# Performance work log

Hardware: AMD Instinct MI355X
Metric: run time of the kernel (lower is better)

The kernel has to match this reference:

```python
import jax, jax.numpy as jnp
import numpy as np

N_NODES = 100000
N_EDGES = 1600000
F_IN, H1, H2 = 128, 64, 32


def spmm(src, dst, edge_weight, x, n_nodes):
    # A @ x with A in COO form: out[dst] += w * x[src]
    msgs = x[src] * edge_weight[:, None]          # [E, d] gather + scale
    return jax.ops.segment_sum(msgs, dst, num_segments=n_nodes)


def setup_inputs() -> dict:
    key = jax.random.key(0)
    k1, k2, k3, k4, k5, k6 = jax.random.split(key, 6)
    features = jax.random.normal(k1, (N_NODES, F_IN), dtype=jnp.float32)
    # positive weights, roughly 1/deg scale as in a normalized adjacency
    edge_weight = jax.random.uniform(k2, (N_EDGES,), dtype=jnp.float32) * 0.125
    W1 = jax.random.normal(k3, (F_IN, H1), dtype=jnp.float32) * (1.0 / np.sqrt(F_IN))
    W2 = jax.random.normal(k4, (H1, H2), dtype=jnp.float32) * (1.0 / np.sqrt(H1))
    src = jax.random.randint(k5, (N_EDGES,), 0, N_NODES, dtype=jnp.int64 if jax.config.jax_enable_x64 else jnp.int32)
    dst = jax.random.randint(k6, (N_EDGES,), 0, N_NODES, dtype=jnp.int64 if jax.config.jax_enable_x64 else jnp.int32)
    return {"features": features, "edge_weight": edge_weight, "W1": W1, "W2": W2,
            "src": src, "dst": dst}


def reference(features, edge_weight, W1, W2, src, dst):
    # Layer 1: relu(A @ (X W1)); dropout is identity (eval mode / rate 0)
    h1 = jax.nn.relu(spmm(src, dst, edge_weight, features @ W1, N_NODES))  # [N, H1]
    # Layer 2: A @ (h1 W2)
    embeddings = spmm(src, dst, edge_weight, h1 @ W2, N_NODES)             # [N, H2]
    return embeddings
```

## Files before the change

### kernel.cpp

```cpp
#include <hip/hip_runtime.h>
#include <hip/hip_fp16.h>


constexpr int N_NODES = 100000;
constexpr int N_EDGES = 1600000;
constexpr int F_IN = 128;
constexpr int H1 = 64;
constexpr int H2 = 32;
constexpr int BSHIFT = 9;
constexpr int BNODES = 1 << BSHIFT;
constexpr int NBUCK = (N_NODES + BNODES - 1) / BNODES;
constexpr int CAP = 10240;
constexpr int CHUNK = 4096;
constexpr int P1_WGS = (N_EDGES + CHUNK - 1) / CHUNK;
constexpr int GEMM_WGS = (N_NODES + 255) / 256;

__global__ __launch_bounds__(256) void init_cursors(int* __restrict__ cursor)
{
    int t = threadIdx.x;
    if (t < NBUCK) cursor[t] = t * CAP;
}

__global__ __launch_bounds__(256) void pass1_bin_gemm1(
    const int* __restrict__ src, const int* __restrict__ dst,
    const float* __restrict__ w, int* __restrict__ cursor,
    int2* __restrict__ staging,
    const float* __restrict__ X, const float* __restrict__ W1,
    __half* __restrict__ xw1out)
{
    __shared__ float smem[F_IN * H1];

    if (blockIdx.x < GEMM_WGS) {
        for (int i = threadIdx.x; i < F_IN * H1; i += 256) smem[i] = W1[i];
        __syncthreads();
        int row = blockIdx.x * 256 + threadIdx.x;
        if (row >= N_NODES) return;
        const float4* xr = reinterpret_cast<const float4*>(X + (size_t)row * F_IN);
        float4 acc[H1 / 4];
#pragma unroll
        for (int j = 0; j < H1 / 4; ++j) acc[j] = make_float4(0.f, 0.f, 0.f, 0.f);
        for (int k4 = 0; k4 < F_IN / 4; ++k4) {
            float4 xv = xr[k4];
#pragma unroll
            for (int kk = 0; kk < 4; ++kk) {
                float xk = (kk == 0) ? xv.x : (kk == 1) ? xv.y
                         : (kk == 2) ? xv.z : xv.w;
                const float4* wr = reinterpret_cast<const float4*>(
                    &smem[(k4 * 4 + kk) * H1]);
#pragma unroll
                for (int j = 0; j < H1 / 4; ++j) {
                    float4 wv = wr[j];
                    acc[j].x += xk * wv.x;
                    acc[j].y += xk * wv.y;
                    acc[j].z += xk * wv.z;
                    acc[j].w += xk * wv.w;
                }
            }
        }
        __half2* oh = reinterpret_cast<__half2*>(xw1out + (size_t)row * H1);
#pragma unroll
        for (int j = 0; j < H1 / 4; ++j) {
            oh[j * 2 + 0] = __floats2half2_rn(acc[j].x, acc[j].y);
            oh[j * 2 + 1] = __floats2half2_rn(acc[j].z, acc[j].w);
        }
        return;
    }

    int* lcnt  = (int*)smem;
    int* lbase = lcnt + 256;

    int e0 = (blockIdx.x - GEMM_WGS) * CHUNK;
    int nhere = N_EDGES - e0; if (nhere > CHUNK) nhere = CHUNK;

    lcnt[threadIdx.x] = 0;
    __syncthreads();

    int   es[16];
    int   ed[16];
    float ew[16];
    {
        bool v = (threadIdx.x * 16) < nhere;
        int tb = e0 + threadIdx.x * 16;
        if (v) {
            const int4* sp = reinterpret_cast<const int4*>(src + tb);
            const int4* dp = reinterpret_cast<const int4*>(dst + tb);
            const float4* wp = reinterpret_cast<const float4*>(w + tb);
#pragma unroll
            for (int q = 0; q < 4; ++q) {
                int4 sv = sp[q], dv = dp[q]; float4 wv = wp[q];
                es[4*q+0]=sv.x; es[4*q+1]=sv.y; es[4*q+2]=sv.z; es[4*q+3]=sv.w;
                ed[4*q+0]=dv.x; ed[4*q+1]=dv.y; ed[4*q+2]=dv.z; ed[4*q+3]=dv.w;
                ew[4*q+0]=wv.x; ew[4*q+1]=wv.y; ew[4*q+2]=wv.z; ew[4*q+3]=wv.w;
            }
        } else {
#pragma unroll
            for (int k = 0; k < 16; ++k) { es[k]=0; ed[k]=-1; ew[k]=0.f; }
        }
    }
#pragma unroll
    for (int k = 0; k < 16; ++k)
        if (ed[k] >= 0) atomicAdd(&lcnt[ed[k] >> BSHIFT], 1);
    __syncthreads();
    if (threadIdx.x < NBUCK) {
        int c = lcnt[threadIdx.x];
        lbase[threadIdx.x] = (c > 0) ? atomicAdd(&cursor[threadIdx.x], c) : 0;
    }
    __syncthreads();
    lcnt[threadIdx.x] = 0;
    __syncthreads();
#pragma unroll
    for (int k = 0; k < 16; ++k) {
        if (ed[k] >= 0) {
            int b = ed[k] >> BSHIFT;
            int r = atomicAdd(&lcnt[b], 1);
            int pos = lbase[b] + r;
            if (pos < (b + 1) * CAP)
                staging[pos] = make_int2(
                    es[k] | ((ed[k] & (BNODES - 1)) << 17),
                    __float_as_int(ew[k]));
        }
    }
}

__global__ __launch_bounds__(1024) void sort_bucket(
    const int* __restrict__ cursor, const int2* __restrict__ staging,
    int2* __restrict__ csr, int2* __restrict__ seg)
{
    __shared__ int  lcnt[BNODES];
    __shared__ int  lofs[BNODES];
    __shared__ int2 sorted[CAP];
    __shared__ int  total_sh;

    int b = blockIdx.x, t = threadIdx.x;
    int base = b * CAP;
    int cnt = cursor[b] - base; if (cnt > CAP) cnt = CAP;

    if (t < BNODES) lcnt[t] = 0;
    __syncthreads();

    for (int j = t; j < cnt; j += 1024)
        atomicAdd(&lcnt[(staging[base + j].x >> 17) & (BNODES - 1)], 1);
    __syncthreads();

    int v = (t < BNODES) ? lcnt[t] : 0;
    int pc = (v + 3) & ~3;
    if (t < BNODES) lofs[t] = pc;
    __syncthreads();
    for (int off = 1; off < BNODES; off <<= 1) {
        int add = (t >= off && t < BNODES) ? lofs[t - off] : 0;
        __syncthreads();
        if (t < BNODES) lofs[t] += add;
        __syncthreads();
    }
    if (t < BNODES) {
        int pexcl = lofs[t] - pc;
        seg[b * BNODES + t] = make_int2(base + pexcl, pc);
        lcnt[t] = pexcl;
        for (int j = v; j < pc; ++j)
            if (pexcl + j < CAP) sorted[pexcl + j] = make_int2(0, 0);
        if (t == BNODES - 1) {
            int tot = lofs[t]; if (tot > CAP) tot = CAP;
            total_sh = tot;
        }
    }
    __syncthreads();

    for (int j = t; j < cnt; j += 1024) {
        int2 c = staging[base + j];
        int node = (c.x >> 17) & (BNODES - 1);
        int pos = atomicAdd(&lcnt[node], 1);
        if (pos < CAP) sorted[pos] = make_int2(c.x & 0x1FFFF, c.y);
    }
    __syncthreads();

    int total = total_sh;
    for (int j = t; j < total; j += 1024) csr[base + j] = sorted[j];
}

__global__ __launch_bounds__(256) void spmm1_fused(
    const int2* __restrict__ seg, const int2* __restrict__ csr,
    const __half* __restrict__ xin, const float* __restrict__ W2,
    __half* __restrict__ h1w2h)
{
    int gid = blockIdx.x * 256 + threadIdx.x;
    int node = __builtin_amdgcn_readfirstlane(gid >> 6);
    int f = gid & 63;
    int par = f >> 5;
    int f2 = f & 31;

    float w2r[32];
#pragma unroll
    for (int kk = 0; kk < 32; ++kk)
        w2r[kk] = W2[(par * 32 + kk) * H2 + f2];

    int2 s = seg[node];
    int start = __builtin_amdgcn_readfirstlane(s.x);
    int cntp  = __builtin_amdgcn_readfirstlane(s.y);
    const int4* csr4 = reinterpret_cast<const int4*>(csr);

    float2 a0 = make_float2(0.f, 0.f), a1 = make_float2(0.f, 0.f);
    for (int e = start; e < start + cntp; e += 4) {
        int4 p0 = csr4[(e >> 1) + 0];
        int4 p1 = csr4[(e >> 1) + 1];
        int  sA = par ? p0.z : p0.x;
        float wA = __int_as_float(par ? p0.w : p0.y);
        int  sB = par ? p1.z : p1.x;
        float wB = __int_as_float(par ? p1.w : p1.y);
        float2 xA = __half22float2(
            *reinterpret_cast<const __half2*>(&xin[(size_t)sA * H1 + 2 * f2]));
        float2 xB = __half22float2(
            *reinterpret_cast<const __half2*>(&xin[(size_t)sB * H1 + 2 * f2]));
        a0.x += wA * xA.x; a0.y += wA * xA.y;
        a1.x += wB * xB.x; a1.y += wB * xB.y;
    }
    float rx = a0.x + a1.x, ry = a0.y + a1.y;
    rx += __shfl_xor(rx, 32, 64);
    ry += __shfl_xor(ry, 32, 64);
    rx = fmaxf(rx, 0.f); ry = fmaxf(ry, 0.f);

    float o = 0.f;
#pragma unroll
    for (int kk = 0; kk < 32; kk += 2) {
        int p = 16 * par + (kk >> 1);
        o += __shfl(rx, p, 64) * w2r[kk];
        o += __shfl(ry, p, 64) * w2r[kk + 1];
    }
    o += __shfl_xor(o, 32, 64);
    if (f < 32)
        h1w2h[(size_t)node * H2 + f2] = __float2half(o);
}

__global__ __launch_bounds__(256) void spmm_csr32h(
    const int2* __restrict__ seg, const int2* __restrict__ csr,
    const __half* __restrict__ xin, float* __restrict__ out)
{
    int gid = blockIdx.x * 256 + threadIdx.x;
    int node = __builtin_amdgcn_readfirstlane(gid >> 6);
    int lane = gid & 63;
    int slot = lane >> 4;
    int f2 = lane & 15;

    int2 s = seg[node];
    int start = __builtin_amdgcn_readfirstlane(s.x);
    int cntp  = __builtin_amdgcn_readfirstlane(s.y);
    int endp = start + cntp;
    const int4* csr4 = reinterpret_cast<const int4*>(csr);

    float2 a0 = make_float2(0.f, 0.f), a1 = make_float2(0.f, 0.f);
    int e = start;
    for (; e + 8 <= endp; e += 8) {
        int4 q0 = csr4[(e >> 1) + 0];
        int4 q1 = csr4[(e >> 1) + 1];
        int4 q2 = csr4[(e >> 1) + 2];
        int4 q3 = csr4[(e >> 1) + 3];
        int4 qa = (slot & 2) ? q1 : q0;
        int  sA = (slot & 1) ? qa.z : qa.x;
        float wA = __int_as_float((slot & 1) ? qa.w : qa.y);
        int4 qb = (slot & 2) ? q3 : q2;
        int  sB = (slot & 1) ? qb.z : qb.x;
        float wB = __int_as_float((slot & 1) ? qb.w : qb.y);
        float2 xA = __half22float2(
            *reinterpret_cast<const __half2*>(&xin[(size_t)sA * H2 + 2 * f2]));
        float2 xB = __half22float2(
            *reinterpret_cast<const __half2*>(&xin[(size_t)sB * H2 + 2 * f2]));
        a0.x += wA * xA.x; a0.y += wA * xA.y;
        a1.x += wB * xB.x; a1.y += wB * xB.y;
    }
    if (e < endp) {
        int4 q0 = csr4[(e >> 1) + 0];
        int4 q1 = csr4[(e >> 1) + 1];
        int4 qa = (slot & 2) ? q1 : q0;
        int  sA = (slot & 1) ? qa.z : qa.x;
        float wA = __int_as_float((slot & 1) ? qa.w : qa.y);
        float2 xA = __half22float2(
            *reinterpret_cast<const __half2*>(&xin[(size_t)sA * H2 + 2 * f2]));
        a0.x += wA * xA.x; a0.y += wA * xA.y;
    }
    float ox = a0.x + a1.x, oy = a0.y + a1.y;
    ox += __shfl_xor(ox, 16, 64); oy += __shfl_xor(oy, 16, 64);
    ox += __shfl_xor(ox, 32, 64); oy += __shfl_xor(oy, 32, 64);
    if (lane < 16)
        *reinterpret_cast<float2*>(&out[(size_t)node * H2 + 2 * f2]) =
            make_float2(ox, oy);
}

extern "C" void kernel_launch(void* const* d_in, const int* in_sizes, int n_in,
                              void* d_out, int out_size, void* d_ws, size_t ws_size,
                              hipStream_t stream)
{
    const float* features    = (const float*)d_in[0];
    const float* edge_weight = (const float*)d_in[1];
    const float* W1          = (const float*)d_in[2];
    const float* W2          = (const float*)d_in[3];
    const int*   src         = (const int*)d_in[4];
    const int*   dst         = (const int*)d_in[5];
    float* out = (float*)d_out;

    char* p = (char*)d_ws;
    __half* xw1h   = (__half*)p;    p += (size_t)N_NODES * H1 * 2;
    __half* h1w2h  = (__half*)p;    p += (size_t)N_NODES * H2 * 2;
    int2*  staging = (int2*)p;      p += (size_t)NBUCK * CAP * 8;
    int2*  csr     = (int2*)p;      p += (size_t)NBUCK * CAP * 8;
    int2*  seg     = (int2*)p;      p += (size_t)NBUCK * BNODES * 8;
    int*   cursor  = (int*)p;       p += 256 * 4;

    init_cursors<<<1, 256, 0, stream>>>(cursor);
    pass1_bin_gemm1<<<P1_WGS + GEMM_WGS, 256, 0, stream>>>(
        src, dst, edge_weight, cursor, staging, features, W1, xw1h);
    sort_bucket<<<NBUCK, 1024, 0, stream>>>(cursor, staging, csr, seg);

    spmm1_fused<<<(N_NODES * 64) / 256, 256, 0, stream>>>(seg, csr, xw1h, W2, h1w2h);
    spmm_csr32h<<<(N_NODES * 64) / 256, 256, 0, stream>>>(seg, csr, h1w2h, out);
}
```

Measured before the change: 158.0 us.

## Restructure layer-1 SpMM into persistent waves with four-edge slots and 8-byte gathers

The fused layer-1 SpMM kernel now runs as a persistent grid of 8192 blocks, where each wave loops over many nodes instead of one wave per node. Inside a wave, lanes split into four edge slots of 16 lanes, and each lane gathers 4 halves (8 bytes) per edge, so 8 edges are processed per iteration instead of 4. A tail path handles leftover edges. The aim is fewer, wider gather loads and an amortised W2 register load, at the cost of an extra cross-slot shuffle reduction and a shuffle-heavy W2 product.

```diff
diff --git a/kernel.cpp b/kernel.cpp
--- a/kernel.cpp
+++ b/kernel.cpp
@@ -14,6 +14,8 @@
 constexpr int CHUNK = 4096;
 constexpr int P1_WGS = (N_EDGES + CHUNK - 1) / CHUNK;
 constexpr int GEMM_WGS = (N_NODES + 255) / 256;
+constexpr int SP1_BLOCKS = 8192;
+constexpr int SP1_WAVES = SP1_BLOCKS * 4;
 
 __global__ __launch_bounds__(256) void init_cursors(int* __restrict__ cursor)
 {
@@ -182,52 +184,84 @@
     const __half* __restrict__ xin, const float* __restrict__ W2,
     __half* __restrict__ h1w2h)
 {
-    int gid = blockIdx.x * 256 + threadIdx.x;
-    int node = __builtin_amdgcn_readfirstlane(gid >> 6);
-    int f = gid & 63;
-    int par = f >> 5;
-    int f2 = f & 31;
+    int tid = blockIdx.x * 256 + threadIdx.x;
+    int wave0 = tid >> 6;
+    int f = tid & 63;
+    int slot = f >> 4;
+    int fq = f & 15;
+    int j = f & 31;
+    int khalf = f >> 5;
+    int shalf = slot >> 1;
+    int spar = slot & 1;
 
     float w2r[32];
 #pragma unroll
     for (int kk = 0; kk < 32; ++kk)
-        w2r[kk] = W2[(par * 32 + kk) * H2 + f2];
-
-    int2 s = seg[node];
-    int start = __builtin_amdgcn_readfirstlane(s.x);
-    int cntp  = __builtin_amdgcn_readfirstlane(s.y);
+        w2r[kk] = W2[(khalf * 32 + kk) * H2 + j];
+
     const int4* csr4 = reinterpret_cast<const int4*>(csr);
 
-    float2 a0 = make_float2(0.f, 0.f), a1 = make_float2(0.f, 0.f);
-    for (int e = start; e < start + cntp; e += 4) {
-        int4 p0 = csr4[(e >> 1) + 0];
-        int4 p1 = csr4[(e >> 1) + 1];
-        int  sA = par ? p0.z : p0.x;
-        float wA = __int_as_float(par ? p0.w : p0.y);
-        int  sB = par ? p1.z : p1.x;
-        float wB = __int_as_float(par ? p1.w : p1.y);
-        float2 xA = __half22float2(
-            *reinterpret_cast<const __half2*>(&xin[(size_t)sA * H1 + 2 * f2]));
-        float2 xB = __half22float2(
-            *reinterpret_cast<const __half2*>(&xin[(size_t)sB * H1 + 2 * f2]));
-        a0.x += wA * xA.x; a0.y += wA * xA.y;
-        a1.x += wB * xB.x; a1.y += wB * xB.y;
-    }
-    float rx = a0.x + a1.x, ry = a0.y + a1.y;
-    rx += __shfl_xor(rx, 32, 64);
-    ry += __shfl_xor(ry, 32, 64);
-    rx = fmaxf(rx, 0.f); ry = fmaxf(ry, 0.f);
-
-    float o = 0.f;
-#pragma unroll
-    for (int kk = 0; kk < 32; kk += 2) {
-        int p = 16 * par + (kk >> 1);
-        o += __shfl(rx, p, 64) * w2r[kk];
-        o += __shfl(ry, p, 64) * w2r[kk + 1];
-    }
-    o += __shfl_xor(o, 32, 64);
-    if (f < 32)
-        h1w2h[(size_t)node * H2 + f2] = __float2half(o);
+    for (int node = wave0; node < N_NODES; node += SP1_WAVES) {
+        int2 s = seg[node];
+        int start = __builtin_amdgcn_readfirstlane(s.x);
+        int cntp  = __builtin_amdgcn_readfirstlane(s.y);
+        int endp = start + cntp;
+
+        float a0 = 0.f, a1 = 0.f, a2 = 0.f, a3 = 0.f;
+        float b0 = 0.f, b1 = 0.f, b2 = 0.f, b3 = 0.f;
+        int e = start;
+        for (; e + 8 <= endp; e += 8) {
+            int4 qa = csr4[(e >> 1) + shalf];
+            int4 qb = csr4[(e >> 1) + 2 + shalf];
+            int  sA = spar ? qa.z : qa.x;
+            float wA = __int_as_float(spar ? qa.w : qa.y);
+            int  sB = spar ? qb.z : qb.x;
+            float wB = __int_as_float(spar ? qb.w : qb.y);
+            uint2 va = *reinterpret_cast<const uint2*>(
+                &xin[(size_t)sA * H1 + 4 * fq]);
+            uint2 vb = *reinterpret_cast<const uint2*>(
+                &xin[(size_t)sB * H1 + 4 * fq]);
+            float2 xa0 = __half22float2(*reinterpret_cast<__half2*>(&va.x));
+            float2 xa1 = __half22float2(*reinterpret_cast<__half2*>(&va.y));
+            float2 xb0 = __half22float2(*reinterpret_cast<__half2*>(&vb.x));
+            float2 xb1 = __half22float2(*reinterpret_cast<__half2*>(&vb.y));
+            a0 += wA * xa0.x; a1 += wA * xa0.y;
+            a2 += wA * xa1.x; a3 += wA * xa1.y;
+            b0 += wB * xb0.x; b1 += wB * xb0.y;
+            b2 += wB * xb1.x; b3 += wB * xb1.y;
+        }
+        if (e < endp) {
+            int4 qa = csr4[(e >> 1) + shalf];
+            int  sA = spar ? qa.z : qa.x;
+            float wA = __int_as_float(spar ? qa.w : qa.y);
+            uint2 va = *reinterpret_cast<const uint2*>(
+                &xin[(size_t)sA * H1 + 4 * fq]);
+            float2 xa0 = __half22float2(*reinterpret_cast<__half2*>(&va.x));
+            float2 xa1 = __half22float2(*reinterpret_cast<__half2*>(&va.y));
+            a0 += wA * xa0.x; a1 += wA * xa0.y;
+            a2 += wA * xa1.x; a3 += wA * xa1.y;
+        }
+        a0 += b0; a1 += b1; a2 += b2; a3 += b3;
+        a0 += __shfl_xor(a0, 16, 64); a1 += __shfl_xor(a1, 16, 64);
+        a2 += __shfl_xor(a2, 16, 64); a3 += __shfl_xor(a3, 16, 64);
+        a0 += __shfl_xor(a0, 32, 64); a1 += __shfl_xor(a1, 32, 64);
+        a2 += __shfl_xor(a2, 32, 64); a3 += __shfl_xor(a3, 32, 64);
+        a0 = fmaxf(a0, 0.f); a1 = fmaxf(a1, 0.f);
+        a2 = fmaxf(a2, 0.f); a3 = fmaxf(a3, 0.f);
+
+        int qbase = 8 * khalf;
+        float o = 0.f;
+#pragma unroll
+        for (int kk = 0; kk < 32; ++kk) {
+            int srcl = qbase + (kk >> 2);
+            float hv = (kk & 3) == 0 ? a0 : (kk & 3) == 1 ? a1
+                     : (kk & 3) == 2 ? a2 : a3;
+            o += __shfl(hv, srcl, 64) * w2r[kk];
+        }
+        o += __shfl_xor(o, 32, 64);
+        if (f < 32)
+            h1w2h[(size_t)node * H2 + j] = __float2half(o);
+    }
 }
 
 __global__ __launch_bounds__(256) void spmm_csr32h(
@@ -309,6 +343,6 @@
         src, dst, edge_weight, cursor, staging, features, W1, xw1h);
     sort_bucket<<<NBUCK, 1024, 0, stream>>>(cursor, staging, csr, seg);
 
-    spmm1_fused<<<(N_NODES * 64) / 256, 256, 0, stream>>>(seg, csr, xw1h, W2, h1w2h);
+    spmm1_fused<<<SP1_BLOCKS, 256, 0, stream>>>(seg, csr, xw1h, W2, h1w2h);
     spmm_csr32h<<<(N_NODES * 64) / 256, 256, 0, stream>>>(seg, csr, h1w2h, out);
 }
```

After: 162.1 us. +2.6%, slower.
